# Optimization experiments

Hardware: AMD Instinct MI355X
Metric: run time of the kernel (lower is better)

The kernel has to match this reference:

```python
import jax, jax.numpy as jnp
import numpy as np

N = 50000        # spots / nodes
D_IN = 3000      # genes
FH1, FH2 = 100, 20
GH1, GH2 = 32, 8
K = 10           # dec_cluster_n
LAT = FH2 + GH2  # 28
E = 800000       # edges
BN_EPS = 1e-4
ALPHA = 1.0


def _xavier_u(k, shape):
    lim = np.sqrt(6.0 / (shape[0] + shape[1])).astype(np.float32)
    return jax.random.uniform(k, shape, jnp.float32, -lim, lim)


def _xavier_n(k, shape):
    std = np.sqrt(2.0 / (shape[0] + shape[1])).astype(np.float32)
    return jax.random.normal(k, shape, jnp.float32) * std


def setup_inputs() -> dict:
    key = jax.random.key(0)
    ks = jax.random.split(key, 16)
    x = jax.random.normal(ks[0], (N, D_IN), jnp.float32)
    edge_row = jax.random.randint(ks[1], (E,), 0, N, jnp.int32)
    edge_col = jax.random.randint(ks[2], (E,), 0, N, jnp.int32)
    adj_vals = jax.random.uniform(ks[3], (E,), jnp.float32)
    return {
        "x": x,
        "adj_vals": adj_vals,
        "enc_W1": _xavier_u(ks[4], (D_IN, FH1)), "enc_b1": jnp.zeros((FH1,), jnp.float32),
        "bn1_g": jnp.ones((FH1,), jnp.float32), "bn1_b": jnp.zeros((FH1,), jnp.float32),
        "enc_W2": _xavier_u(ks[5], (FH1, FH2)), "enc_b2": jnp.zeros((FH2,), jnp.float32),
        "bn2_g": jnp.ones((FH2,), jnp.float32), "bn2_b": jnp.zeros((FH2,), jnp.float32),
        "gc1_W": _xavier_u(ks[6], (FH2, GH1)),
        "gc2_W": _xavier_u(ks[7], (GH1, GH2)),
        "gc3_W": _xavier_u(ks[8], (GH1, GH2)),
        "dec_W": _xavier_u(ks[9], (LAT, D_IN)), "dec_b": jnp.zeros((D_IN,), jnp.float32),
        "bn3_g": jnp.ones((D_IN,), jnp.float32), "bn3_b": jnp.zeros((D_IN,), jnp.float32),
        "cluster": _xavier_n(ks[10], (K, LAT)),
        "edge_row": edge_row, "edge_col": edge_col,
    }


def _full_block(h, W, b, g, bb):
    # Linear -> BatchNorm(eval: running_mean=0, running_var=1) -> ELU (dropout off in eval)
    h = h @ W + b
    h = h * (g * jax.lax.rsqrt(jnp.float32(1.0 + BN_EPS))) + bb
    return jax.nn.elu(h)


def _spmm(vals, row, col, dense):
    # sparse (COO) adjacency @ dense: gather source rows, scale, scatter-add to dest
    return jax.ops.segment_sum(vals[:, None] * dense[col], row, num_segments=N)


def reference(x, adj_vals, enc_W1, enc_b1, bn1_g, bn1_b, enc_W2, enc_b2, bn2_g, bn2_b,
              gc1_W, gc2_W, gc3_W, dec_W, dec_b, bn3_g, bn3_b, cluster,
              edge_row, edge_col):
    # encoder MLP
    feat_x = _full_block(x, enc_W1, enc_b1, bn1_g, bn1_b)          # [N, FH1]
    feat_x = _full_block(feat_x, enc_W2, enc_b2, bn2_g, bn2_b)     # [N, FH2]
    # GCN layers (eval: dropout identity)
    h1 = jax.nn.relu(_spmm(adj_vals, edge_row, edge_col, feat_x @ gc1_W))  # [N, GH1]
    mu = _spmm(adj_vals, edge_row, edge_col, h1 @ gc2_W)           # [N, GH2]
    logvar = _spmm(adj_vals, edge_row, edge_col, h1 @ gc3_W)       # [N, GH2]
    gnn_z = mu                                                     # reparameterize in eval = mu
    z = jnp.concatenate([feat_x, gnn_z], axis=1)                   # [N, LAT]
    de_feat = _full_block(z, dec_W, dec_b, bn3_g, bn3_b)           # [N, D_IN]
    # DEC soft assignment (Student-t, alpha=1 => exponent (alpha+1)/2 = 1)
    dist = jnp.sum(jnp.square(z[:, None, :] - cluster[None, :, :]), axis=2)  # [N, K]
    q = 1.0 / (1.0 + dist / ALPHA)
    q = q / jnp.sum(q, axis=1, keepdims=True)
    return (z, mu, logvar, de_feat, q, feat_x, gnn_z)
```

## Files before the change

kernel.cpp:

```cpp
#include <hip/hip_runtime.h>
#include <math.h>

#define NROWS 50000
#define DIN   3000
#define FH1   100
#define FH2   20
#define GH1   32
#define GH2   8
#define KCL   10
#define LAT   28
#define NEDGE 800000

static __device__ __forceinline__ float elu1(float v) {
  return v > 0.f ? v : (__expf(v) - 1.f);
}

static __device__ __forceinline__ unsigned short f2bf(float f) {
  unsigned int u = __float_as_uint(f);
  unsigned int r = (u + 0x7FFFu + ((u >> 16) & 1u)) >> 16;
  return (unsigned short)r;
}

#define BN_RS 0.99995000374968754f

typedef __attribute__((ext_vector_type(8))) short bf16x8_t;
typedef __attribute__((ext_vector_type(4))) float f32x4_t;

#define GLL(gp, lp)                                                              \
  __builtin_amdgcn_global_load_lds(                                              \
      (const __attribute__((address_space(1))) void*)(gp),                       \
      (__attribute__((address_space(3))) void*)(lp), 16, 0, 0)

__global__ __launch_bounds__(256) void k_prepW(const float* __restrict__ W,
                                               unsigned short* __restrict__ Wt) {
  const int idx = blockIdx.x * 256 + threadIdx.x;
  const int n = idx / 376;
  const int kc = (idx - n * 376) * 8;
  if (n >= 112) return;
  unsigned short v[8];
#pragma unroll
  for (int j = 0; j < 8; ++j) {
    const int k = kc + j;
    const float f = (n < FH1 && k < DIN) ? W[(size_t)k * FH1 + n] : 0.f;
    v[j] = f2bf(f);
  }
  uint4 pv;
  pv.x = (unsigned)v[0] | ((unsigned)v[1] << 16);
  pv.y = (unsigned)v[2] | ((unsigned)v[3] << 16);
  pv.z = (unsigned)v[4] | ((unsigned)v[5] << 16);
  pv.w = (unsigned)v[6] | ((unsigned)v[7] << 16);
  *(uint4*)&Wt[(size_t)n * 3008 + kc] = pv;
}

__global__ __launch_bounds__(256) void k_gemm1(
    const float* __restrict__ x, const unsigned short* __restrict__ Wt,
    const float* __restrict__ b1, const float* __restrict__ g1, const float* __restrict__ bb1,
    float* __restrict__ out)
{
  __shared__ float Af[2 * 4096];
  __shared__ unsigned short Bf[2 * 7168];

  const int tid = threadIdx.x;
  const int w = tid >> 6, lane = tid & 63;
  const int fr = lane & 15;
  const int fk = (lane >> 4) * 8;
  const int rowBase = blockIdx.x * 64;

  f32x4_t acc[7];
#pragma unroll
  for (int f = 0; f < 7; ++f) acc[f] = (f32x4_t){0.f, 0.f, 0.f, 0.f};

#define STAGE_A(bb, tt)                                                          \
  {                                                                              \
    _Pragma("unroll")                                                            \
    for (int i = 0; i < 4; ++i) {                                                \
      const int c_ = w * 4 + i;                                                  \
      const int rl_ = c_ * 4 + (lane >> 4);                                      \
      const int v_ = lane & 15;                                                  \
      const int u_ = (v_ & 8) | ((v_ ^ rl_) & 7);                                \
      const int rg_ = (rowBase + rl_ < NROWS) ? rowBase + rl_ : (NROWS - 1);     \
      GLL(x + (size_t)rg_ * DIN + (tt) * 64 + u_ * 4,                            \
          (char*)&Af[(bb) * 4096] + c_ * 1024);                                  \
    }                                                                            \
  }
#define STAGE_B(bb, tt)                                                          \
  {                                                                              \
    _Pragma("unroll")                                                            \
    for (int i = 0; i < 4; ++i) {                                                \
      const int c_ = w + i * 4;                                                  \
      if (c_ < 14) {                                                             \
        const int n_ = c_ * 8 + (lane >> 3);                                     \
        const int vb_ = lane & 7;                                                \
        const int ub_ = vb_ ^ (n_ & 7);                                          \
        GLL(Wt + (size_t)n_ * 3008 + (tt) * 64 + ub_ * 8,                        \
            (char*)&Bf[(bb) * 7168] + c_ * 1024);                                \
      }                                                                          \
    }                                                                            \
  }
#define STAGE_A_TAIL(bb)                                                         \
  {                                                                              \
    _Pragma("unroll")                                                            \
    for (int j = 0; j < 4; ++j) {                                                \
      const int idx_ = tid * 4 + j;                                              \
      const int r_ = idx_ >> 4;                                                  \
      const int u_ = idx_ & 15;                                                  \
      const int kk_ = 2944 + u_ * 4;                                             \
      const int rg_ = (rowBase + r_ < NROWS) ? rowBase + r_ : (NROWS - 1);       \
      float4 val_ = make_float4(0.f, 0.f, 0.f, 0.f);                             \
      if (kk_ + 3 < DIN) val_ = *(const float4*)&x[(size_t)rg_ * DIN + kk_];     \
      const int v_ = (u_ & 8) | ((u_ ^ r_) & 7);                                 \
      *(float4*)&Af[(bb) * 4096 + r_ * 64 + v_ * 4] = val_;                      \
    }                                                                            \
  }

  STAGE_A(0, 0)
  STAGE_B(0, 0)
  __syncthreads();

  const int r = w * 16 + fr;
  int cur = 0;

  for (int t = 0; t < 47; ++t) {
    if (t < 46) {
      if (t + 1 == 46) { STAGE_A_TAIL(cur ^ 1) } else { STAGE_A(cur ^ 1, t + 1) }
      STAGE_B(cur ^ 1, t + 1)
    }

    const float* Ab = &Af[cur * 4096 + r * 64];
    bf16x8_t a[2];
#pragma unroll
    for (int h = 0; h < 2; ++h) {
      const int u0 = h * 8 + (fk >> 2);
      const int u1 = u0 + 1;
      const int v0 = (u0 & 8) | ((u0 ^ r) & 7);
      const int v1 = (u1 & 8) | ((u1 ^ r) & 7);
      const float4 p = *(const float4*)&Ab[v0 * 4];
      const float4 q = *(const float4*)&Ab[v1 * 4];
      uint4 av;
      av.x = (unsigned)f2bf(p.x) | ((unsigned)f2bf(p.y) << 16);
      av.y = (unsigned)f2bf(p.z) | ((unsigned)f2bf(p.w) << 16);
      av.z = (unsigned)f2bf(q.x) | ((unsigned)f2bf(q.y) << 16);
      av.w = (unsigned)f2bf(q.z) | ((unsigned)f2bf(q.w) << 16);
      a[h] = *(const bf16x8_t*)&av;
    }
#pragma unroll
    for (int f = 0; f < 7; ++f) {
      const int n = f * 16 + fr;
      const int ub0 = (fk >> 3);
#pragma unroll
      for (int h = 0; h < 2; ++h) {
        const int vb = (h * 4 + ub0) ^ (n & 7);
        const bf16x8_t b = *(const bf16x8_t*)&Bf[cur * 7168 + n * 64 + vb * 8];
        acc[f] = __builtin_amdgcn_mfma_f32_16x16x32_bf16(a[h], b, acc[f], 0, 0, 0);
      }
    }

    __syncthreads();
    cur ^= 1;
  }
#undef STAGE_A
#undef STAGE_B
#undef STAGE_A_TAIL

  const int s4 = (lane >> 4) * 4;
#pragma unroll
  for (int f = 0; f < 7; ++f) {
    const int col = f * 16 + fr;
    if (col < FH1) {
      const float sc = g1[col] * BN_RS;
      const float bbv = bb1[col];
      const float bv = b1[col];
#pragma unroll
      for (int j = 0; j < 4; ++j) {
        const int row = rowBase + w * 16 + s4 + j;
        if (row < NROWS)
          out[(size_t)row * FH1 + col] = elu1((acc[f][j] + bv) * sc + bbv);
      }
    }
  }
}

__global__ __launch_bounds__(256) void k_enc2_gc1(
    const float* __restrict__ feat1, const float* __restrict__ W2, const float* __restrict__ b2,
    const float* __restrict__ g2, const float* __restrict__ bb2,
    const float* __restrict__ gc1W,
    float* __restrict__ fx_out, float* __restrict__ t1_out)
{
  const int row = blockIdx.x * blockDim.x + threadIdx.x;
  if (row >= NROWS) return;
  float f1[FH1];
  const float4* fr = (const float4*)(feat1 + (size_t)row * FH1);
#pragma unroll
  for (int i = 0; i < FH1/4; ++i) ((float4*)f1)[i] = fr[i];

  float fx[FH2];
#pragma unroll
  for (int j = 0; j < FH2; ++j) fx[j] = b2[j];
#pragma unroll
  for (int k = 0; k < FH1; ++k) {
    const float f = f1[k];
#pragma unroll
    for (int j = 0; j < FH2; ++j) fx[j] = fmaf(f, W2[k*FH2 + j], fx[j]);
  }
#pragma unroll
  for (int j = 0; j < FH2; ++j) fx[j] = elu1(fx[j] * (g2[j] * BN_RS) + bb2[j]);

  float4* fo = (float4*)(fx_out + (size_t)row * FH2);
#pragma unroll
  for (int i = 0; i < FH2/4; ++i) fo[i] = ((float4*)fx)[i];

  float t[GH1];
#pragma unroll
  for (int j = 0; j < GH1; ++j) t[j] = 0.f;
#pragma unroll
  for (int k = 0; k < FH2; ++k) {
    const float f = fx[k];
#pragma unroll
    for (int j = 0; j < GH1; ++j) t[j] = fmaf(f, gc1W[k*GH1 + j], t[j]);
  }
  float4* to = (float4*)(t1_out + (size_t)row * GH1);
#pragma unroll
  for (int i = 0; i < GH1/4; ++i) to[i] = ((float4*)t)[i];
}

__global__ void k_zero_i(int* __restrict__ p, int n) {
  for (int i = blockIdx.x * blockDim.x + threadIdx.x; i < n; i += gridDim.x * blockDim.x)
    p[i] = 0;
}

__global__ void k_hist(const int* __restrict__ er, int* __restrict__ deg) {
  const int e = blockIdx.x * 256 + threadIdx.x;
  if (e < NEDGE) atomicAdd(&deg[er[e]], 1);
}

__global__ __launch_bounds__(1024) void k_scan(const int* __restrict__ deg,
                                               int* __restrict__ start) {
  __shared__ int sm[1024];
  const int t = threadIdx.x;
  const int c0 = t * 49;
  const int c1 = (c0 + 49 < NROWS) ? c0 + 49 : NROWS;
  int s = 0;
  for (int i = c0; i < c1; ++i) s += deg[i];
  sm[t] = s;
  __syncthreads();
  for (int off = 1; off < 1024; off <<= 1) {
    int v = (t >= off) ? sm[t - off] : 0;
    __syncthreads();
    sm[t] += v;
    __syncthreads();
  }
  int run = (t == 0) ? 0 : sm[t - 1];
  for (int i = c0; i < c1; ++i) { start[i] = run; run += deg[i]; }
  if (t == 0) start[NROWS] = NEDGE;
}

__global__ void k_scatter(const int* __restrict__ er, const int* __restrict__ ec,
                          const float* __restrict__ vals, const int* __restrict__ start,
                          int* __restrict__ cnt, int* __restrict__ colS,
                          float* __restrict__ valS) {
  const int e = blockIdx.x * 256 + threadIdx.x;
  if (e >= NEDGE) return;
  const int r = er[e];
  const int pos = start[r] + atomicAdd(&cnt[r], 1);
  colS[pos] = ec[e];
  valS[pos] = vals[e];
}

__global__ __launch_bounds__(256) void k_spmm1g(
    const int* __restrict__ start, const int* __restrict__ colS, const float* __restrict__ valS,
    const float* __restrict__ t1, float* __restrict__ h1)
{
  const int tid = threadIdx.x;
  const int row = blockIdx.x * 32 + (tid >> 3);
  const int p = tid & 7;
  if (row >= NROWS) return;
  const int s = start[row], e = start[row + 1];
  float4 acc = make_float4(0.f, 0.f, 0.f, 0.f);
  for (int j = s; j < e; ++j) {
    const int c = colS[j];
    const float v = valS[j];
    const float4 tv = *(const float4*)&t1[(size_t)c * GH1 + p * 4];
    acc.x = fmaf(v, tv.x, acc.x);
    acc.y = fmaf(v, tv.y, acc.y);
    acc.z = fmaf(v, tv.z, acc.z);
    acc.w = fmaf(v, tv.w, acc.w);
  }
  *(float4*)&h1[(size_t)row * GH1 + p * 4] = acc;
}

__global__ __launch_bounds__(256) void k_h1gc(
    const float* __restrict__ h1, const float* __restrict__ gc2W, const float* __restrict__ gc3W,
    float* __restrict__ mp, float* __restrict__ lp)
{
  const int row = blockIdx.x * blockDim.x + threadIdx.x;
  if (row >= NROWS) return;
  float h[GH1];
  const float4* hr = (const float4*)(h1 + (size_t)row * GH1);
#pragma unroll
  for (int i = 0; i < GH1/4; ++i) ((float4*)h)[i] = hr[i];
#pragma unroll
  for (int k = 0; k < GH1; ++k) h[k] = fmaxf(h[k], 0.f);

  float m[GH2], l[GH2];
#pragma unroll
  for (int j = 0; j < GH2; ++j) { m[j] = 0.f; l[j] = 0.f; }
#pragma unroll
  for (int k = 0; k < GH1; ++k) {
    const float hv = h[k];
#pragma unroll
    for (int j = 0; j < GH2; ++j) {
      m[j] = fmaf(hv, gc2W[k*GH2 + j], m[j]);
      l[j] = fmaf(hv, gc3W[k*GH2 + j], l[j]);
    }
  }
  float4* mo = (float4*)(mp + (size_t)row * GH2);
  float4* lo = (float4*)(lp + (size_t)row * GH2);
  mo[0] = ((float4*)m)[0]; mo[1] = ((float4*)m)[1];
  lo[0] = ((float4*)l)[0]; lo[1] = ((float4*)l)[1];
}

__global__ __launch_bounds__(256) void k_spmm2g(
    const int* __restrict__ start, const int* __restrict__ colS, const float* __restrict__ valS,
    const float* __restrict__ mp, const float* __restrict__ lp,
    float* __restrict__ mu, float* __restrict__ lv)
{
  const int tid = threadIdx.x;
  const int row = blockIdx.x * 64 + (tid >> 2);
  const int p = tid & 3;
  if (row >= NROWS) return;
  const float* src = (p < 2) ? mp : lp;
  float* dst = (p < 2) ? mu : lv;
  const int off = (p & 1) * 4;
  const int s = start[row], e = start[row + 1];
  float4 acc = make_float4(0.f, 0.f, 0.f, 0.f);
  for (int j = s; j < e; ++j) {
    const int c = colS[j];
    const float v = valS[j];
    const float4 sv = *(const float4*)&src[(size_t)c * GH2 + off];
    acc.x = fmaf(v, sv.x, acc.x);
    acc.y = fmaf(v, sv.y, acc.y);
    acc.z = fmaf(v, sv.z, acc.z);
    acc.w = fmaf(v, sv.w, acc.w);
  }
  *(float4*)&dst[(size_t)row * GH2 + off] = acc;
}

__global__ __launch_bounds__(256) void k_zq(
    const float* __restrict__ fx, const float* __restrict__ mu, const float* __restrict__ clus,
    float* __restrict__ z_o, float* __restrict__ gz_o, float* __restrict__ q_o)
{
  const int row = blockIdx.x * blockDim.x + threadIdx.x;
  if (row >= NROWS) return;
  float z[LAT];
  const float4* f4 = (const float4*)(fx + (size_t)row * FH2);
#pragma unroll
  for (int i = 0; i < FH2/4; ++i) ((float4*)z)[i] = f4[i];
  const float4* m4 = (const float4*)(mu + (size_t)row * GH2);
  ((float4*)z)[5] = m4[0];
  ((float4*)z)[6] = m4[1];

  float4* zo = (float4*)(z_o + (size_t)row * LAT);
#pragma unroll
  for (int i = 0; i < LAT/4; ++i) zo[i] = ((float4*)z)[i];
  float4* go = (float4*)(gz_o + (size_t)row * GH2);
  go[0] = m4[0]; go[1] = m4[1];

  float q[KCL];
  float ssum = 0.f;
#pragma unroll
  for (int j = 0; j < KCL; ++j) {
    float d = 0.f;
#pragma unroll
    for (int k = 0; k < LAT; ++k) {
      const float df = z[k] - clus[j*LAT + k];
      d = fmaf(df, df, d);
    }
    q[j] = 1.f / (1.f + d);
    ssum += q[j];
  }
  const float inv = 1.f / ssum;
#pragma unroll
  for (int j = 0; j < KCL; ++j) q[j] *= inv;
  float2* qo = (float2*)(q_o + (size_t)row * KCL);
#pragma unroll
  for (int i = 0; i < KCL/2; ++i) qo[i] = ((float2*)q)[i];
}

__global__ __launch_bounds__(256) void k_dec(
    const float* __restrict__ z, const float* __restrict__ W, const float* __restrict__ db,
    const float* __restrict__ g3, const float* __restrict__ bb3, float* __restrict__ out)
{
  __shared__ float Ws[LAT][256];
  __shared__ float zs[16 * LAT];

  const int tid = threadIdx.x;
  const int c0  = blockIdx.x * 256;
  const int r0  = blockIdx.y * 16;

#pragma unroll
  for (int rep = 0; rep < 7; ++rep) {
    const int f4 = rep * 256 + tid;
    const int k  = f4 >> 6;
    const int cg = (f4 & 63) * 4;
    float4 v = make_float4(0.f, 0.f, 0.f, 0.f);
    if (c0 + cg < DIN) v = *(const float4*)&W[(size_t)k * DIN + c0 + cg];
    *(float4*)&Ws[k][cg] = v;
  }
  if (tid < 112) {
    *(float4*)&zs[tid * 4] = *(const float4*)&z[(size_t)r0 * LAT + tid * 4];
  }
  __syncthreads();

  const int w    = tid >> 6;
  const int lane = tid & 63;
  const int cl   = lane * 4;
  const int rloc = w * 4;

  float acc[4][4];
#pragma unroll
  for (int i = 0; i < 4; ++i)
#pragma unroll
    for (int j = 0; j < 4; ++j) acc[i][j] = 0.f;

#pragma unroll
  for (int k4 = 0; k4 < 7; ++k4) {
    float zq[4][4];
#pragma unroll
    for (int i = 0; i < 4; ++i)
      *(float4*)zq[i] = *(const float4*)&zs[(rloc + i) * LAT + k4 * 4];
#pragma unroll
    for (int kk = 0; kk < 4; ++kk) {
      const float4 wv = *(const float4*)&Ws[k4 * 4 + kk][cl];
#pragma unroll
      for (int i = 0; i < 4; ++i) {
        acc[i][0] = fmaf(zq[i][kk], wv.x, acc[i][0]);
        acc[i][1] = fmaf(zq[i][kk], wv.y, acc[i][1]);
        acc[i][2] = fmaf(zq[i][kk], wv.z, acc[i][2]);
        acc[i][3] = fmaf(zq[i][kk], wv.w, acc[i][3]);
      }
    }
  }

  if (c0 + cl >= DIN) return;
  const float4 db4 = *(const float4*)&db[c0 + cl];
  const float4 g4  = *(const float4*)&g3[c0 + cl];
  const float4 bb4 = *(const float4*)&bb3[c0 + cl];
#pragma unroll
  for (int i = 0; i < 4; ++i) {
    float4 v;
    v.x = elu1((acc[i][0] + db4.x) * (g4.x * BN_RS) + bb4.x);
    v.y = elu1((acc[i][1] + db4.y) * (g4.y * BN_RS) + bb4.y);
    v.z = elu1((acc[i][2] + db4.z) * (g4.z * BN_RS) + bb4.z);
    v.w = elu1((acc[i][3] + db4.w) * (g4.w * BN_RS) + bb4.w);
    *(float4*)&out[(size_t)(r0 + rloc + i) * DIN + c0 + cl] = v;
  }
}

extern "C" void kernel_launch(void* const* d_in, const int* in_sizes, int n_in,
                              void* d_out, int out_size, void* d_ws, size_t ws_size,
                              hipStream_t stream) {
  const float* x    = (const float*)d_in[0];
  const float* vals = (const float*)d_in[1];
  const float* W1   = (const float*)d_in[2];
  const float* b1   = (const float*)d_in[3];
  const float* g1   = (const float*)d_in[4];
  const float* bb1  = (const float*)d_in[5];
  const float* W2   = (const float*)d_in[6];
  const float* b2   = (const float*)d_in[7];
  const float* g2   = (const float*)d_in[8];
  const float* bb2  = (const float*)d_in[9];
  const float* gc1W = (const float*)d_in[10];
  const float* gc2W = (const float*)d_in[11];
  const float* gc3W = (const float*)d_in[12];
  const float* dW   = (const float*)d_in[13];
  const float* db   = (const float*)d_in[14];
  const float* g3   = (const float*)d_in[15];
  const float* bb3  = (const float*)d_in[16];
  const float* clus = (const float*)d_in[17];
  const int* erow   = (const int*)d_in[18];
  const int* ecol   = (const int*)d_in[19];

  float* out  = (float*)d_out;
  float* z_o  = out;
  float* mu_o = out + (size_t)NROWS * 28;
  float* lv_o = out + (size_t)NROWS * 36;
  float* de_o = out + (size_t)NROWS * 44;
  float* q_o  = out + (size_t)NROWS * 3044;
  float* fx_o = out + (size_t)NROWS * 3054;
  float* gz_o = out + (size_t)NROWS * 3074;

  float* feat1 = de_o;
  float* t1    = de_o + (size_t)NROWS * 100;
  float* h1    = de_o + (size_t)NROWS * 132;
  float* mp    = de_o + (size_t)NROWS * 164;
  float* lp    = de_o + (size_t)NROWS * 172;
  unsigned short* Wt = (unsigned short*)(de_o + (size_t)NROWS * 200);
  int*   deg   = (int*)(de_o + (size_t)NROWS * 210);
  int*   cnt   = (int*)(de_o + (size_t)NROWS * 211);
  int*   startA= (int*)(de_o + (size_t)NROWS * 212);
  int*   colS  = (int*)(de_o + (size_t)NROWS * 214);
  float* valS  = de_o + (size_t)NROWS * 230;

  k_prepW<<<dim3(165), 256, 0, stream>>>(W1, Wt);
  k_gemm1<<<dim3(782), 256, 0, stream>>>(x, Wt, b1, g1, bb1, feat1);
  k_enc2_gc1<<<dim3((NROWS + 255) / 256), 256, 0, stream>>>(feat1, W2, b2, g2, bb2, gc1W, fx_o, t1);

  k_zero_i<<<dim3(128), 256, 0, stream>>>(deg, 2 * NROWS);
  k_hist<<<dim3((NEDGE + 255) / 256), 256, 0, stream>>>(erow, deg);
  k_scan<<<dim3(1), 1024, 0, stream>>>(deg, startA);
  k_scatter<<<dim3((NEDGE + 255) / 256), 256, 0, stream>>>(erow, ecol, vals, startA, cnt, colS, valS);

  k_spmm1g<<<dim3((NROWS + 31) / 32), 256, 0, stream>>>(startA, colS, valS, t1, h1);
  k_h1gc<<<dim3((NROWS + 255) / 256), 256, 0, stream>>>(h1, gc2W, gc3W, mp, lp);
  k_spmm2g<<<dim3((NROWS + 63) / 64), 256, 0, stream>>>(startA, colS, valS, mp, lp, mu_o, lv_o);
  k_zq<<<dim3((NROWS + 255) / 256), 256, 0, stream>>>(fx_o, mu_o, clus, z_o, gz_o, q_o);
  k_dec<<<dim3(12, 3125), 256, 0, stream>>>(z_o, dW, db, g3, bb3, de_o);
}
```

Measured before the change: 655.8 us.

## Compute decoder GEMM with bf16 MFMA using prepacked transposed weights

The decoder GEMM (z[N,28] x W[28,3000]) moves from an FP32 shared-memory kernel to a bf16 MFMA 16x16x32 kernel. It reads z directly, converts it to bf16 in registers, and reads a prepacked column-major bf16 copy of the decoder weights. The packed weights sit in the de_feat output region, so the row blocks that overlap that scratch space (213-214) are skipped in the MFMA pass and recomputed afterwards by the old FP32 kernel. The aim is to cut ALU work in this output-write-dominated kernel, at the cost of bf16 rounding on the decoder outputs.

```diff
diff --git a/kernel.cpp b/kernel.cpp
--- a/kernel.cpp
+++ b/kernel.cpp
@@ -50,6 +50,27 @@
   pv.z = (unsigned)v[4] | ((unsigned)v[5] << 16);
   pv.w = (unsigned)v[6] | ((unsigned)v[7] << 16);
   *(uint4*)&Wt[(size_t)n * 3008 + kc] = pv;
+}
+
+__global__ __launch_bounds__(256) void k_prepDec(const float* __restrict__ W,
+                                                 unsigned short* __restrict__ Wd) {
+  const int idx = blockIdx.x * 256 + threadIdx.x;
+  const int col = idx >> 2;
+  const int kc = (idx & 3) * 8;
+  if (col >= 3072) return;
+  unsigned short v[8];
+#pragma unroll
+  for (int j = 0; j < 8; ++j) {
+    const int k = kc + j;
+    const float f = (col < DIN && k < LAT) ? W[(size_t)k * DIN + col] : 0.f;
+    v[j] = f2bf(f);
+  }
+  uint4 pv;
+  pv.x = (unsigned)v[0] | ((unsigned)v[1] << 16);
+  pv.y = (unsigned)v[2] | ((unsigned)v[3] << 16);
+  pv.z = (unsigned)v[4] | ((unsigned)v[5] << 16);
+  pv.w = (unsigned)v[6] | ((unsigned)v[7] << 16);
+  *(uint4*)&Wd[(size_t)col * 32 + kc] = pv;
 }
 
 __global__ __launch_bounds__(256) void k_gemm1(
@@ -386,7 +407,56 @@
   for (int i = 0; i < KCL/2; ++i) qo[i] = ((float2*)q)[i];
 }
 
-__global__ __launch_bounds__(256) void k_dec(
+__global__ __launch_bounds__(256) void k_decm(
+    const float* __restrict__ z, const unsigned short* __restrict__ Wd,
+    const float* __restrict__ db, const float* __restrict__ g3, const float* __restrict__ bb3,
+    float* __restrict__ out)
+{
+  const int yb = blockIdx.y;
+  if (yb == 213 || yb == 214) return;
+  const int tid = threadIdx.x;
+  const int w = tid >> 6, lane = tid & 63;
+  const int fr = lane & 15;
+  const int g = lane >> 4;
+  const int fk = g * 8;
+  const int r0 = yb * 16;
+  const int c0w = blockIdx.x * 256 + w * 64;
+
+  const float* zp = z + (size_t)(r0 + fr) * LAT;
+  float4 p = make_float4(0.f, 0.f, 0.f, 0.f), q = p;
+  if (g < 3) {
+    p = *(const float4*)&zp[fk];
+    q = *(const float4*)&zp[fk + 4];
+  } else {
+    p = *(const float4*)&zp[24];
+  }
+  uint4 av;
+  av.x = (unsigned)f2bf(p.x) | ((unsigned)f2bf(p.y) << 16);
+  av.y = (unsigned)f2bf(p.z) | ((unsigned)f2bf(p.w) << 16);
+  av.z = (unsigned)f2bf(q.x) | ((unsigned)f2bf(q.y) << 16);
+  av.w = (unsigned)f2bf(q.z) | ((unsigned)f2bf(q.w) << 16);
+  const bf16x8_t a = *(const bf16x8_t*)&av;
+
+#pragma unroll
+  for (int nf = 0; nf < 4; ++nf) {
+    const int col = c0w + nf * 16 + fr;
+    const uint4 bv = *(const uint4*)&Wd[(size_t)col * 32 + fk];
+    f32x4_t acc = (f32x4_t){0.f, 0.f, 0.f, 0.f};
+    acc = __builtin_amdgcn_mfma_f32_16x16x32_bf16(a, *(const bf16x8_t*)&bv, acc, 0, 0, 0);
+    if (col < DIN) {
+      const float sc = g3[col] * BN_RS;
+      const float bbv = bb3[col];
+      const float dbv = db[col];
+#pragma unroll
+      for (int j = 0; j < 4; ++j) {
+        const int row = r0 + g * 4 + j;
+        out[(size_t)row * DIN + col] = elu1((acc[j] + dbv) * sc + bbv);
+      }
+    }
+  }
+}
+
+__global__ __launch_bounds__(256) void k_dect(
     const float* __restrict__ z, const float* __restrict__ W, const float* __restrict__ db,
     const float* __restrict__ g3, const float* __restrict__ bb3, float* __restrict__ out)
 {
@@ -395,7 +465,7 @@
 
   const int tid = threadIdx.x;
   const int c0  = blockIdx.x * 256;
-  const int r0  = blockIdx.y * 16;
+  const int r0  = (blockIdx.y + 213) * 16;
 
 #pragma unroll
   for (int rep = 0; rep < 7; ++rep) {
@@ -495,6 +565,7 @@
   float* mp    = de_o + (size_t)NROWS * 164;
   float* lp    = de_o + (size_t)NROWS * 172;
   unsigned short* Wt = (unsigned short*)(de_o + (size_t)NROWS * 200);
+  unsigned short* Wd = (unsigned short*)(de_o + (size_t)3408 * DIN);
   int*   deg   = (int*)(de_o + (size_t)NROWS * 210);
   int*   cnt   = (int*)(de_o + (size_t)NROWS * 211);
   int*   startA= (int*)(de_o + (size_t)NROWS * 212);
@@ -502,6 +573,7 @@
   float* valS  = de_o + (size_t)NROWS * 230;
 
   k_prepW<<<dim3(165), 256, 0, stream>>>(W1, Wt);
+  k_prepDec<<<dim3(48), 256, 0, stream>>>(dW, Wd);
   k_gemm1<<<dim3(782), 256, 0, stream>>>(x, Wt, b1, g1, bb1, feat1);
   k_enc2_gc1<<<dim3((NROWS + 255) / 256), 256, 0, stream>>>(feat1, W2, b2, g2, bb2, gc1W, fx_o, t1);
 
@@ -514,5 +586,6 @@
   k_h1gc<<<dim3((NROWS + 255) / 256), 256, 0, stream>>>(h1, gc2W, gc3W, mp, lp);
   k_spmm2g<<<dim3((NROWS + 63) / 64), 256, 0, stream>>>(startA, colS, valS, mp, lp, mu_o, lv_o);
   k_zq<<<dim3((NROWS + 255) / 256), 256, 0, stream>>>(fx_o, mu_o, clus, z_o, gz_o, q_o);
-  k_dec<<<dim3(12, 3125), 256, 0, stream>>>(z_o, dW, db, g3, bb3, de_o);
-}
+  k_decm<<<dim3(12, 3125), 256, 0, stream>>>(z_o, Wd, db, g3, bb3, de_o);
+  k_dect<<<dim3(12, 2), 256, 0, stream>>>(z_o, dW, db, g3, bb3, de_o);
+}
```

New measurement: 678.6 us. +3.5%, slower.
